# Kernel tuning notes

Hardware: AMD Instinct MI355X
Metric: run time of the kernel (lower is better)

Reference implementation:

```python
import jax, jax.numpy as jnp
import numpy as np

N, T, E = 20000, 4, 320000
IN_F, H_F, OUT_F, HEADS = 32, 16, 16, 8
NEG_SLOPE = 0.2


def gat_layer(x, W, al, ar, b, src, dst, n_nodes, heads, f_out):
    # x: [N, T, Fin], W: [Fin, heads*f_out], al/ar: [heads, f_out], b: [heads*f_out]
    feat = (x @ W).reshape(x.shape[0], x.shape[1], heads, f_out)      # [N,T,H,F]
    el = (feat * al).sum(-1)                                          # [N,T,H]
    er = (feat * ar).sum(-1)                                          # [N,T,H]
    e = jax.nn.leaky_relu(el[src] + er[dst], NEG_SLOPE)               # [E,T,H]
    # segment softmax over incoming edges of each destination node
    m = jax.lax.stop_gradient(jax.ops.segment_max(e, dst, num_segments=n_nodes))
    ex = jnp.exp(e - m[dst])
    s = jax.ops.segment_sum(ex, dst, num_segments=n_nodes)
    alpha = ex / s[dst]                                               # [E,T,H]
    msg = feat[src] * alpha[..., None]                                # [E,T,H,F]
    out = jax.ops.segment_sum(msg, dst, num_segments=n_nodes)
    return out + b.reshape(1, 1, heads, f_out)


def setup_inputs() -> dict:
    key = jax.random.key(0)
    ks = jax.random.split(key, 12)
    x = jax.random.normal(ks[0], (N, T, IN_F), dtype=jnp.float32)
    src = jax.random.randint(ks[1], (E,), 0, N)
    dst = jax.random.randint(ks[2], (E,), 0, N)
    s = 0.1
    W1 = jax.random.normal(ks[3], (IN_F, HEADS * H_F), dtype=jnp.float32) * s
    al1 = jax.random.normal(ks[4], (HEADS, H_F), dtype=jnp.float32) * s
    ar1 = jax.random.normal(ks[5], (HEADS, H_F), dtype=jnp.float32) * s
    b1 = jnp.zeros((HEADS * H_F,), dtype=jnp.float32)
    W2 = jax.random.normal(ks[6], (HEADS * H_F, OUT_F), dtype=jnp.float32) * s
    al2 = jax.random.normal(ks[7], (1, OUT_F), dtype=jnp.float32) * s
    ar2 = jax.random.normal(ks[8], (1, OUT_F), dtype=jnp.float32) * s
    b2 = jnp.zeros((OUT_F,), dtype=jnp.float32)
    return {"x": x, "src": src, "dst": dst, "W1": W1, "al1": al1, "ar1": ar1,
            "b1": b1, "W2": W2, "al2": al2, "ar2": ar2, "b2": b2}


def reference(x, src, dst, W1, al1, ar1, b1, W2, al2, ar2, b2):
    n = x.shape[0]
    h = gat_layer(x, W1, al1, ar1, b1, src, dst, n, HEADS, H_F)   # [N,T,H,F]
    h = h.reshape(n, h.shape[1], -1)                              # [N,T,H*F]
    h = gat_layer(h, W2, al2, ar2, b2, src, dst, n, 1, OUT_F)     # [N,T,1,OUT]
    return h.squeeze(2)                                           # [N,T,OUT]
```

## Files before the change

kernel.cpp:

```cpp
#include <hip/hip_runtime.h>
#include <hip/hip_fp16.h>
#include <math.h>

#define NN 20000
#define TT 4
#define EE 320000
#define NT (NN*TT)
#define H1 8
#define C1 128
#define IN_F 32
#define OUT_F 16
#define CAP 96
#define SCAT_BLOCKS 313
#define XCAST_BLOCKS 1250

typedef _Float16 h8 __attribute__((ext_vector_type(8)));
typedef float f32x4 __attribute__((ext_vector_type(4)));

__device__ __forceinline__ float lrelu_exp(float e) {
  e = (e >= 0.f) ? e : 0.2f * e;
  return __expf(e);
}

__global__ __launch_bounds__(256) void k_front(
    const float* __restrict__ x, const float* __restrict__ W1,
    const float* __restrict__ al1, const float* __restrict__ ar1,
    const float* __restrict__ W2, const float* __restrict__ al2,
    const float* __restrict__ ar2,
    const int4* __restrict__ src4, const int4* __restrict__ dst4,
    int* __restrict__ cnt, int* __restrict__ csr96,
    __half* __restrict__ xh, float* __restrict__ el1, float* __restrict__ er1,
    __half* __restrict__ W1hp, __half* __restrict__ W2pp) {
  __shared__ h8 ELERs[64];
  int b = blockIdx.x;
  int tid = threadIdx.x;
  if (b < SCAT_BLOCKS) {
    int e4 = b * 256 + tid;
    if (e4 < EE / 4) {
      int4 s = src4[e4];
      int4 d = dst4[e4];
      int p0 = atomicAdd(&cnt[d.x], 1); csr96[d.x * CAP + p0] = s.x;
      int p1 = atomicAdd(&cnt[d.y], 1); csr96[d.y * CAP + p1] = s.y;
      int p2 = atomicAdd(&cnt[d.z], 1); csr96[d.z * CAP + p2] = s.z;
      int p3 = atomicAdd(&cnt[d.w], 1); csr96[d.w * CAP + p3] = s.w;
    }
    return;
  }
  if (b == SCAT_BLOCKS) {
    for (int idx = tid; idx < 8 * 512; idx += 256) {
      int tile = idx >> 9;
      int rem = idx & 511;
      int lane = rem >> 3, j = rem & 7;
      int k = (lane >> 4) * 8 + j;
      int n = lane & 15;
      W1hp[idx] = __float2half(W1[k * C1 + tile * 16 + n]);
    }
    for (int idx = tid; idx < 8 * 512; idx += 256) {
      int tile = idx >> 9;
      int rem = idx & 511;
      int lane = rem >> 3, j = rem & 7;
      int ks = tile & 3;
      int k = ks * 32 + (lane >> 4) * 8 + j;
      int n = lane & 15;
      float v = 0.f;
      if (tile < 4) {
        v = W2[k * OUT_F + n];
      } else if (n == 0) {
        float s = 0.f;
        for (int f = 0; f < 16; ++f) s += W2[k * OUT_F + f] * al2[f];
        v = s;
      } else if (n == 1) {
        float s = 0.f;
        for (int f = 0; f < 16; ++f) s += W2[k * OUT_F + f] * ar2[f];
        v = s;
      }
      W2pp[idx] = __float2half(v);
    }
    return;
  }
  {
    __half* E = (__half*)ELERs;
    for (int idx = tid; idx < 512; idx += 256) {
      int lane = idx >> 3, j = idx & 7;
      int k = (lane >> 4) * 8 + j;
      int n = lane & 15;
      int hh_ = n & 7;
      const float* a = (n < 8) ? al1 : ar1;
      float s = 0.f;
      for (int f = 0; f < 16; ++f) s += W1[k * C1 + hh_ * 16 + f] * a[hh_ * 16 + f];
      E[idx] = __float2half(s);
    }
  }
  __syncthreads();
  int wave = tid >> 6, lane = tid & 63;
  int m = lane & 15, quad = lane >> 4;
  int rowbase = (b - SCAT_BLOCKS - 1) * 64 + wave * 16;
  int row = rowbase + m;
  const float4* xp = (const float4*)(x + row * IN_F + quad * 8);
  float4 a0 = xp[0], a1 = xp[1];
  h8 af;
  af[0] = (_Float16)a0.x; af[1] = (_Float16)a0.y;
  af[2] = (_Float16)a0.z; af[3] = (_Float16)a0.w;
  af[4] = (_Float16)a1.x; af[5] = (_Float16)a1.y;
  af[6] = (_Float16)a1.z; af[7] = (_Float16)a1.w;
  *(h8*)(xh + (size_t)row * IN_F + quad * 8) = af;
  {
    h8 bf = ELERs[lane];
    f32x4 c = {0.f, 0.f, 0.f, 0.f};
    c = __builtin_amdgcn_mfma_f32_16x16x32_f16(af, bf, c, 0, 0, 0);
#pragma unroll
    for (int r = 0; r < 4; ++r) {
      int orow = rowbase + quad * 4 + r;
      if (m < 8) el1[orow * H1 + m] = c[r];
      else       er1[orow * H1 + (m - 8)] = c[r];
    }
  }
}

__global__ __launch_bounds__(256) void k_agg1m(
    const __half* __restrict__ xh,
    const float* __restrict__ el1,
    const float* __restrict__ er1,
    const int* __restrict__ cnt, const int* __restrict__ csr96,
    const __half* __restrict__ W1hp, const float* __restrict__ b1,
    const __half* __restrict__ W2pp,
    __half* __restrict__ feat2h, float* __restrict__ el2,
    float* __restrict__ er2) {
  __shared__ __half axs[16][264];
  __shared__ __half hs[16][136];
  int tid = threadIdx.x;
  int wv = tid >> 6, lane = tid & 63;
  int n = blockIdx.x * 4 + wv;
  int slot = lane >> 1;
  int t = lane >> 4;
  int hf = lane & 1;
  float er_i = er1[(size_t)n * 32 + slot];
  int deg = cnt[n];
  const int* eb = csr96 + (size_t)n * CAP;
  h8 accA = {0, 0, 0, 0, 0, 0, 0, 0};
  h8 accB = {0, 0, 0, 0, 0, 0, 0, 0};
  float l = 0.f;
  for (int chunk = 0; chunk < deg; chunk += 64) {
    int m = min(64, deg - chunk);
    int sv = (lane < m) ? eb[chunk + lane] : 0;
    int iters = (m + 3) >> 2;
    for (int g = 0; g < iters; ++g) {
      int j = g * 4;
      int s0 = __builtin_amdgcn_readlane(sv, j + 0);
      int s1 = __builtin_amdgcn_readlane(sv, j + 1);
      int s2 = __builtin_amdgcn_readlane(sv, j + 2);
      int s3 = __builtin_amdgcn_readlane(sv, j + 3);
      float ew0 = el1[(size_t)s0 * 32 + slot];
      float ew1 = el1[(size_t)s1 * 32 + slot];
      float ew2 = el1[(size_t)s2 * 32 + slot];
      float ew3 = el1[(size_t)s3 * 32 + slot];
      const __half* x0 = xh + (size_t)(s0 * 4 + t) * 32 + hf * 16;
      const __half* x1 = xh + (size_t)(s1 * 4 + t) * 32 + hf * 16;
      const __half* x2 = xh + (size_t)(s2 * 4 + t) * 32 + hf * 16;
      const __half* x3 = xh + (size_t)(s3 * 4 + t) * 32 + hf * 16;
      h8 a0 = *(const h8*)x0, b0 = *(const h8*)(x0 + 8);
      h8 a1 = *(const h8*)x1, b1_ = *(const h8*)(x1 + 8);
      h8 a2 = *(const h8*)x2, b2_ = *(const h8*)(x2 + 8);
      h8 a3 = *(const h8*)x3, b3_ = *(const h8*)(x3 + 8);
#define CONSUME(K, EW, XA, XB)                                    \
      {                                                           \
        float w_ = lrelu_exp(EW + er_i);                          \
        w_ = (j + K < m) ? w_ : 0.f;                              \
        l += w_;                                                  \
        _Float16 wh_ = (_Float16)w_;                              \
        h8 w8_ = {wh_, wh_, wh_, wh_, wh_, wh_, wh_, wh_};        \
        accA += w8_ * XA;                                         \
        accB += w8_ * XB;                                         \
      }
      CONSUME(0, ew0, a0, b0) CONSUME(1, ew1, a1, b1_)
      CONSUME(2, ew2, a2, b2_) CONSUME(3, ew3, a3, b3_)
#undef CONSUME
    }
  }
  float inv = (l > 0.f) ? (1.f / l) : 0.f;
  {
    h8 r0, r1;
#pragma unroll
    for (int q = 0; q < 8; ++q) {
      r0[q] = (_Float16)((float)accA[q] * inv);
      r1[q] = (_Float16)((float)accB[q] * inv);
    }
    int hh_ = slot & 7;
    __half* op = &axs[wv * 4 + t][hh_ * 32 + hf * 16];
    *(h8*)op = r0;
    *(h8*)(op + 8) = r1;
  }
  __syncthreads();

  int m = lane & 15, quad = lane >> 4;
  const h8* bp1 = (const h8*)W1hp;
#pragma unroll
  for (int hi = 0; hi < 2; ++hi) {
    int head = wv * 2 + hi;
    h8 af = *(const h8*)&axs[m][head * 32 + quad * 8];
    f32x4 c = {0.f, 0.f, 0.f, 0.f};
    c = __builtin_amdgcn_mfma_f32_16x16x32_f16(af, bp1[head * 64 + lane], c, 0, 0, 0);
    float bv = b1[head * 16 + m];
#pragma unroll
    for (int r = 0; r < 4; ++r)
      hs[quad * 4 + r][head * 16 + m] = __float2half(c[r] + bv);
  }
  __syncthreads();
  if (wv != 0) return;
  const h8* bp2 = (const h8*)W2pp;
  f32x4 cF = {0.f, 0.f, 0.f, 0.f};
  f32x4 cE = {0.f, 0.f, 0.f, 0.f};
#pragma unroll
  for (int ks = 0; ks < 4; ++ks) {
    h8 af = *(const h8*)&hs[m][ks * 32 + quad * 8];
    cF = __builtin_amdgcn_mfma_f32_16x16x32_f16(af, bp2[ks * 64 + lane], cF, 0, 0, 0);
    cE = __builtin_amdgcn_mfma_f32_16x16x32_f16(af, bp2[(4 + ks) * 64 + lane], cE, 0, 0, 0);
  }
#pragma unroll
  for (int r = 0; r < 4; ++r) {
    int orow = blockIdx.x * 16 + quad * 4 + r;
    feat2h[(size_t)orow * OUT_F + m] = __float2half(cF[r]);
    if (m == 0) el2[orow] = cE[r];
    if (m == 1) er2[orow] = cE[r];
  }
}

__global__ __launch_bounds__(256, 4) void k_agg2x(
    const __half* __restrict__ feat2h,
    const float* __restrict__ el2, const float* __restrict__ er2,
    const int* __restrict__ cnt, const int* __restrict__ csr96,
    const float* __restrict__ b2, float* __restrict__ out) {
  __shared__ int4 stg4[4][192];
  int tid = threadIdx.x;
  int wv = tid >> 6, lane = tid & 63;
  int n = blockIdx.x * 4 + wv;
  int t = lane >> 4, f = lane & 15;
  float ern = er2[n * 4 + t];
  int deg = cnt[n];
  const int* eb = csr96 + (size_t)n * CAP;
  const char* f2b = (const char*)feat2h;
  const char* e2b = (const char*)el2;
  char* myst = (char*)stg4[wv];
  float acc = 0.f, l = 0.f;
  for (int chunk = 0; chunk < deg; chunk += 64) {
    int m64 = min(64, deg - chunk);
    int sv = (lane < m64) ? eb[chunk + lane] : 0;
    int nq = (m64 + 15) >> 4;
    for (int q = 0; q < nq; ++q) {
      int mc = min(16, m64 - q * 16);
      int4 st[3];
#pragma unroll
      for (int i = 0; i < 3; ++i) {
        int g = i * 64 + lane;
        int e = g / 9;
        int seg = g - e * 9;
        if (e > 15) { e = 15; seg = 8; }
        int ec = (e < mc) ? e : (mc - 1);
        int s = __builtin_amdgcn_ds_bpermute(((q << 4) + ec) << 2, sv);
        const char* p = (seg < 8)
            ? (f2b + (size_t)s * 128 + seg * 16)
            : (e2b + (size_t)s * 16);
        st[i] = *(const int4*)p;
      }
#pragma unroll
      for (int i = 0; i < 3; ++i)
        *(int4*)(myst + i * 1024 + lane * 16) = st[i];
#pragma unroll
      for (int e = 0; e < 16; ++e) {
        float ew = *(const float*)(myst + e * 144 + 128 + t * 4);
        __half fv = *(const __half*)(myst + e * 144 + t * 32 + f * 2);
        float w_ = lrelu_exp(ew + ern);
        w_ = (e < mc) ? w_ : 0.f;
        l += w_;
        acc = fmaf(w_, __half2float(fv), acc);
      }
    }
  }
  float inv = (l > 0.f) ? (1.f / l) : 0.f;
  out[(size_t)(n * 4 + t) * OUT_F + f] = acc * inv + b2[f];
}

extern "C" void kernel_launch(void* const* d_in, const int* in_sizes, int n_in,
                              void* d_out, int out_size, void* d_ws, size_t ws_size,
                              hipStream_t stream) {
  const float* x   = (const float*)d_in[0];
  const int*   src = (const int*)d_in[1];
  const int*   dst = (const int*)d_in[2];
  const float* W1  = (const float*)d_in[3];
  const float* al1 = (const float*)d_in[4];
  const float* ar1 = (const float*)d_in[5];
  const float* b1  = (const float*)d_in[6];
  const float* W2  = (const float*)d_in[7];
  const float* al2 = (const float*)d_in[8];
  const float* ar2 = (const float*)d_in[9];
  const float* b2  = (const float*)d_in[10];
  float* out = (float*)d_out;

  char* w = (char*)d_ws;
  __half* xh     = (__half*)w; w += (size_t)NT * IN_F * 2;
  __half* feat2h = (__half*)w; w += (size_t)NT * OUT_F * 2;
  float*  el1    = (float*)w;  w += (size_t)NT * H1 * 4;
  float*  er1    = (float*)w;  w += (size_t)NT * H1 * 4;
  float*  el2    = (float*)w;  w += (size_t)NT * 4;
  float*  er2    = (float*)w;  w += (size_t)NT * 4;
  __half* W1hp   = (__half*)w; w += (size_t)8 * 512 * 2;
  __half* W2pp   = (__half*)w; w += (size_t)8 * 512 * 2;
  int* cnt     = (int*)w;      w += (size_t)NN * 4;
  int* csr96   = (int*)w;      w += (size_t)NN * CAP * 4;

  hipMemsetAsync(cnt, 0, NN * sizeof(int), stream);

  k_front<<<SCAT_BLOCKS + 1 + XCAST_BLOCKS, 256, 0, stream>>>(
      x, W1, al1, ar1, W2, al2, ar2, (const int4*)src, (const int4*)dst,
      cnt, csr96, xh, el1, er1, W1hp, W2pp);
  k_agg1m<<<NN / 4, 256, 0, stream>>>(xh, el1, er1, cnt, csr96,
                                      W1hp, b1, W2pp, feat2h, el2, er2);
  k_agg2x<<<NN / 4, 256, 0, stream>>>(feat2h, el2, er2, cnt, csr96, b2, out);
}
```

Before: 150.6 us.

## Double-buffer neighbor gathers in both aggregation kernels; drop LDS staging in agg2

The layer-1 aggregation loop now uses two register sets so the gathers for the next group of four neighbours are issued before the current group is consumed. The layer-2 aggregation kernel drops its shared-memory staging (bpermute plus int4 loads written to LDS) and instead does direct per-lane gathers of el2 and feat2h, eight neighbours per group, with the same two-set register double-buffering. Its occupancy hint in the launch bounds is also removed. The goal is to hide gather latency across iterations, at the cost of more registers and narrower, less coalesced scalar half loads in layer 2.

```diff
diff --git a/kernel.cpp b/kernel.cpp
--- a/kernel.cpp
+++ b/kernel.cpp
@@ -144,38 +144,59 @@
     int m = min(64, deg - chunk);
     int sv = (lane < m) ? eb[chunk + lane] : 0;
     int iters = (m + 3) >> 2;
-    for (int g = 0; g < iters; ++g) {
-      int j = g * 4;
-      int s0 = __builtin_amdgcn_readlane(sv, j + 0);
-      int s1 = __builtin_amdgcn_readlane(sv, j + 1);
-      int s2 = __builtin_amdgcn_readlane(sv, j + 2);
-      int s3 = __builtin_amdgcn_readlane(sv, j + 3);
-      float ew0 = el1[(size_t)s0 * 32 + slot];
-      float ew1 = el1[(size_t)s1 * 32 + slot];
-      float ew2 = el1[(size_t)s2 * 32 + slot];
-      float ew3 = el1[(size_t)s3 * 32 + slot];
-      const __half* x0 = xh + (size_t)(s0 * 4 + t) * 32 + hf * 16;
-      const __half* x1 = xh + (size_t)(s1 * 4 + t) * 32 + hf * 16;
-      const __half* x2 = xh + (size_t)(s2 * 4 + t) * 32 + hf * 16;
-      const __half* x3 = xh + (size_t)(s3 * 4 + t) * 32 + hf * 16;
-      h8 a0 = *(const h8*)x0, b0 = *(const h8*)(x0 + 8);
-      h8 a1 = *(const h8*)x1, b1_ = *(const h8*)(x1 + 8);
-      h8 a2 = *(const h8*)x2, b2_ = *(const h8*)(x2 + 8);
-      h8 a3 = *(const h8*)x3, b3_ = *(const h8*)(x3 + 8);
-#define CONSUME(K, EW, XA, XB)                                    \
-      {                                                           \
-        float w_ = lrelu_exp(EW + er_i);                          \
-        w_ = (j + K < m) ? w_ : 0.f;                              \
-        l += w_;                                                  \
-        _Float16 wh_ = (_Float16)w_;                              \
-        h8 w8_ = {wh_, wh_, wh_, wh_, wh_, wh_, wh_, wh_};        \
-        accA += w8_ * XA;                                         \
-        accB += w8_ * XB;                                         \
-      }
-      CONSUME(0, ew0, a0, b0) CONSUME(1, ew1, a1, b1_)
-      CONSUME(2, ew2, a2, b2_) CONSUME(3, ew3, a3, b3_)
-#undef CONSUME
-    }
+    float ewA0, ewA1, ewA2, ewA3, ewB0, ewB1, ewB2, ewB3;
+    h8 xaA0, xaA1, xaA2, xaA3, xbA0, xbA1, xbA2, xbA3;
+    h8 xaB0, xaB1, xaB2, xaB3, xbB0, xbB1, xbB2, xbB3;
+#define LOADG(S, G)                                                       \
+    {                                                                     \
+      int j_ = (G) * 4;                                                   \
+      int s0 = __builtin_amdgcn_readlane(sv, j_ + 0);                     \
+      int s1 = __builtin_amdgcn_readlane(sv, j_ + 1);                     \
+      int s2 = __builtin_amdgcn_readlane(sv, j_ + 2);                     \
+      int s3 = __builtin_amdgcn_readlane(sv, j_ + 3);                     \
+      ew##S##0 = el1[(size_t)s0 * 32 + slot];                             \
+      ew##S##1 = el1[(size_t)s1 * 32 + slot];                             \
+      ew##S##2 = el1[(size_t)s2 * 32 + slot];                             \
+      ew##S##3 = el1[(size_t)s3 * 32 + slot];                             \
+      const __half* x0 = xh + (size_t)(s0 * 4 + t) * 32 + hf * 16;        \
+      const __half* x1 = xh + (size_t)(s1 * 4 + t) * 32 + hf * 16;        \
+      const __half* x2 = xh + (size_t)(s2 * 4 + t) * 32 + hf * 16;        \
+      const __half* x3 = xh + (size_t)(s3 * 4 + t) * 32 + hf * 16;        \
+      xa##S##0 = *(const h8*)x0; xb##S##0 = *(const h8*)(x0 + 8);         \
+      xa##S##1 = *(const h8*)x1; xb##S##1 = *(const h8*)(x1 + 8);         \
+      xa##S##2 = *(const h8*)x2; xb##S##2 = *(const h8*)(x2 + 8);         \
+      xa##S##3 = *(const h8*)x3; xb##S##3 = *(const h8*)(x3 + 8);         \
+    }
+#define CONS1(JK, EW, XA, XB)                                             \
+    {                                                                     \
+      float w_ = lrelu_exp(EW + er_i);                                    \
+      w_ = ((JK) < m) ? w_ : 0.f;                                         \
+      l += w_;                                                            \
+      _Float16 wh_ = (_Float16)w_;                                        \
+      h8 w8_ = {wh_, wh_, wh_, wh_, wh_, wh_, wh_, wh_};                  \
+      accA += w8_ * XA;                                                   \
+      accB += w8_ * XB;                                                   \
+    }
+#define CONSG(S, G)                                                       \
+    {                                                                     \
+      int j_ = (G) * 4;                                                   \
+      CONS1(j_ + 0, ew##S##0, xa##S##0, xb##S##0)                         \
+      CONS1(j_ + 1, ew##S##1, xa##S##1, xb##S##1)                         \
+      CONS1(j_ + 2, ew##S##2, xa##S##2, xb##S##2)                         \
+      CONS1(j_ + 3, ew##S##3, xa##S##3, xb##S##3)                         \
+    }
+    LOADG(A, 0)
+    int g = 0;
+    for (; g + 1 < iters; g += 2) {
+      LOADG(B, g + 1)
+      CONSG(A, g)
+      if (g + 2 < iters) LOADG(A, g + 2)
+      CONSG(B, g + 1)
+    }
+    if (g < iters) CONSG(A, g)
+#undef LOADG
+#undef CONS1
+#undef CONSG
   }
   float inv = (l > 0.f) ? (1.f / l) : 0.f;
   {
@@ -225,12 +246,11 @@
   }
 }
 
-__global__ __launch_bounds__(256, 4) void k_agg2x(
+__global__ __launch_bounds__(256) void k_agg2x(
     const __half* __restrict__ feat2h,
     const float* __restrict__ el2, const float* __restrict__ er2,
     const int* __restrict__ cnt, const int* __restrict__ csr96,
     const float* __restrict__ b2, float* __restrict__ out) {
-  __shared__ int4 stg4[4][192];
   int tid = threadIdx.x;
   int wv = tid >> 6, lane = tid & 63;
   int n = blockIdx.x * 4 + wv;
@@ -238,43 +258,74 @@
   float ern = er2[n * 4 + t];
   int deg = cnt[n];
   const int* eb = csr96 + (size_t)n * CAP;
-  const char* f2b = (const char*)feat2h;
-  const char* e2b = (const char*)el2;
-  char* myst = (char*)stg4[wv];
   float acc = 0.f, l = 0.f;
   for (int chunk = 0; chunk < deg; chunk += 64) {
-    int m64 = min(64, deg - chunk);
-    int sv = (lane < m64) ? eb[chunk + lane] : 0;
-    int nq = (m64 + 15) >> 4;
-    for (int q = 0; q < nq; ++q) {
-      int mc = min(16, m64 - q * 16);
-      int4 st[3];
-#pragma unroll
-      for (int i = 0; i < 3; ++i) {
-        int g = i * 64 + lane;
-        int e = g / 9;
-        int seg = g - e * 9;
-        if (e > 15) { e = 15; seg = 8; }
-        int ec = (e < mc) ? e : (mc - 1);
-        int s = __builtin_amdgcn_ds_bpermute(((q << 4) + ec) << 2, sv);
-        const char* p = (seg < 8)
-            ? (f2b + (size_t)s * 128 + seg * 16)
-            : (e2b + (size_t)s * 16);
-        st[i] = *(const int4*)p;
-      }
-#pragma unroll
-      for (int i = 0; i < 3; ++i)
-        *(int4*)(myst + i * 1024 + lane * 16) = st[i];
-#pragma unroll
-      for (int e = 0; e < 16; ++e) {
-        float ew = *(const float*)(myst + e * 144 + 128 + t * 4);
-        __half fv = *(const __half*)(myst + e * 144 + t * 32 + f * 2);
-        float w_ = lrelu_exp(ew + ern);
-        w_ = (e < mc) ? w_ : 0.f;
-        l += w_;
-        acc = fmaf(w_, __half2float(fv), acc);
-      }
-    }
+    int m = min(64, deg - chunk);
+    int sv = (lane < m) ? eb[chunk + lane] : 0;
+    int iters = (m + 7) >> 3;
+    float eA0, eA1, eA2, eA3, eA4, eA5, eA6, eA7;
+    float eB0, eB1, eB2, eB3, eB4, eB5, eB6, eB7;
+    __half hA0, hA1, hA2, hA3, hA4, hA5, hA6, hA7;
+    __half hB0, hB1, hB2, hB3, hB4, hB5, hB6, hB7;
+#define LOADG2(S, G)                                                      \
+    {                                                                     \
+      int j_ = (G) * 8;                                                   \
+      int s0 = __builtin_amdgcn_readlane(sv, j_ + 0);                     \
+      int s1 = __builtin_amdgcn_readlane(sv, j_ + 1);                     \
+      int s2 = __builtin_amdgcn_readlane(sv, j_ + 2);                     \
+      int s3 = __builtin_amdgcn_readlane(sv, j_ + 3);                     \
+      int s4 = __builtin_amdgcn_readlane(sv, j_ + 4);                     \
+      int s5 = __builtin_amdgcn_readlane(sv, j_ + 5);                     \
+      int s6 = __builtin_amdgcn_readlane(sv, j_ + 6);                     \
+      int s7 = __builtin_amdgcn_readlane(sv, j_ + 7);                     \
+      e##S##0 = el2[s0 * 4 + t];                                          \
+      e##S##1 = el2[s1 * 4 + t];                                          \
+      e##S##2 = el2[s2 * 4 + t];                                          \
+      e##S##3 = el2[s3 * 4 + t];                                          \
+      e##S##4 = el2[s4 * 4 + t];                                          \
+      e##S##5 = el2[s5 * 4 + t];                                          \
+      e##S##6 = el2[s6 * 4 + t];                                          \
+      e##S##7 = el2[s7 * 4 + t];                                          \
+      h##S##0 = feat2h[(size_t)(s0 * 4 + t) * OUT_F + f];                 \
+      h##S##1 = feat2h[(size_t)(s1 * 4 + t) * OUT_F + f];                 \
+      h##S##2 = feat2h[(size_t)(s2 * 4 + t) * OUT_F + f];                 \
+      h##S##3 = feat2h[(size_t)(s3 * 4 + t) * OUT_F + f];                 \
+      h##S##4 = feat2h[(size_t)(s4 * 4 + t) * OUT_F + f];                 \
+      h##S##5 = feat2h[(size_t)(s5 * 4 + t) * OUT_F + f];                 \
+      h##S##6 = feat2h[(size_t)(s6 * 4 + t) * OUT_F + f];                 \
+      h##S##7 = feat2h[(size_t)(s7 * 4 + t) * OUT_F + f];                 \
+    }
+#define CONS2(JK, EW, FV)                                                 \
+    {                                                                     \
+      float w_ = lrelu_exp(EW + ern);                                     \
+      w_ = ((JK) < m) ? w_ : 0.f;                                         \
+      l += w_;                                                            \
+      acc = fmaf(w_, __half2float(FV), acc);                              \
+    }
+#define CONSG2(S, G)                                                      \
+    {                                                                     \
+      int j_ = (G) * 8;                                                   \
+      CONS2(j_ + 0, e##S##0, h##S##0)                                     \
+      CONS2(j_ + 1, e##S##1, h##S##1)                                     \
+      CONS2(j_ + 2, e##S##2, h##S##2)                                     \
+      CONS2(j_ + 3, e##S##3, h##S##3)                                     \
+      CONS2(j_ + 4, e##S##4, h##S##4)                                     \
+      CONS2(j_ + 5, e##S##5, h##S##5)                                     \
+      CONS2(j_ + 6, e##S##6, h##S##6)                                     \
+      CONS2(j_ + 7, e##S##7, h##S##7)                                     \
+    }
+    LOADG2(A, 0)
+    int g = 0;
+    for (; g + 1 < iters; g += 2) {
+      LOADG2(B, g + 1)
+      CONSG2(A, g)
+      if (g + 2 < iters) LOADG2(A, g + 2)
+      CONSG2(B, g + 1)
+    }
+    if (g < iters) CONSG2(A, g)
+#undef LOADG2
+#undef CONS2
+#undef CONSG2
   }
   float inv = (l > 0.f) ? (1.f / l) : 0.f;
   out[(size_t)(n * 4 + t) * OUT_F + f] = acc * inv + b2[f];
```

Result: slower. 166.0 us (+10.2%).
